# Performance work log

Measured on AMD Instinct MI355X. Metric: run time of the kernel, lower is better.

Reference implementation:

```python
import jax, jax.numpy as jnp
import numpy as np
import math

D_MODEL = 1024
NUM_HEADS = 16
D_K = D_MODEL // NUM_HEADS
THETA = 10000.0
CONTEXT_LENGTH = 2048


def _rope_tables(seq_len):
    # freqs: [d_k/2]
    powers = jnp.arange(0, D_K, 2, dtype=jnp.float32) / D_K
    freqs = 1.0 / (THETA ** powers)
    t = jnp.arange(seq_len, dtype=jnp.float32)
    fm = jnp.outer(t, freqs)  # [s, d_k/2]
    return jnp.cos(fm), jnp.sin(fm)


def _apply_rope(x, cos, sin):
    # x: [b, h, s, d_k]; cos/sin: [s, d_k/2] broadcast to [1,1,s,d_k/2]
    c = cos[None, None, :, :].astype(x.dtype)
    s_ = sin[None, None, :, :].astype(x.dtype)
    xe = x[..., 0::2]
    xo = x[..., 1::2]
    oe = xe * c - xo * s_
    oo = xe * s_ + xo * c
    # interleave even/odd back
    out = jnp.stack([oe, oo], axis=-1).reshape(x.shape)
    return out


def setup_inputs() -> dict:
    key = jax.random.key(0)
    ks = jax.random.split(key, 5)
    b, s = 4, 2048
    std = (2.0 / (D_MODEL + D_MODEL)) ** 0.5
    x = jax.random.normal(ks[0], (b, s, D_MODEL), dtype=jnp.float32)
    Wq = jax.random.normal(ks[1], (D_MODEL, D_MODEL), dtype=jnp.float32) * std
    Wk = jax.random.normal(ks[2], (D_MODEL, D_MODEL), dtype=jnp.float32) * std
    Wv = jax.random.normal(ks[3], (D_MODEL, D_MODEL), dtype=jnp.float32) * std
    Wo = jax.random.normal(ks[4], (D_MODEL, D_MODEL), dtype=jnp.float32) * std
    return {"x": x, "Wq": Wq, "Wk": Wk, "Wv": Wv, "Wo": Wo}


def reference(x, Wq, Wk, Wv, Wo):
    b, s, d = x.shape
    h, dk = NUM_HEADS, D_K
    # projections: Linear applies x @ W.T via einsum('...i,oi->...o')
    def proj(W):
        y = jnp.einsum('bsi,oi->bso', x, W)
        return y.reshape(b, s, h, dk).transpose(0, 2, 1, 3)  # [b,h,s,dk]
    q, k, v = proj(Wq), proj(Wk), proj(Wv)
    cos, sin = _rope_tables(s)
    q = _apply_rope(q, cos, sin)
    k = _apply_rope(k, cos, sin)
    scores = jnp.einsum('bhnd,bhmd->bhnm', q, k) / math.sqrt(dk)
    causal = jnp.tril(jnp.ones((s, s), dtype=bool))
    scores = jnp.where(causal, scores, -jnp.inf)
    probs = jax.nn.softmax(scores, axis=-1)
    attn = jnp.einsum('bhnm,bhmd->bhnd', probs, v)
    attn = attn.transpose(0, 2, 1, 3).reshape(b, s, d)  # [b,s,d_model]
    return jnp.einsum('bsi,oi->bso', attn, Wo)
```

## Files before the change

kernel.cpp:

```cpp
#include <hip/hip_runtime.h>
#include <hip/hip_bf16.h>
#include <math.h>

typedef __attribute__((ext_vector_type(4))) float f32x4;
typedef __attribute__((ext_vector_type(16))) float f32x16;
typedef __attribute__((ext_vector_type(8))) short s16x8;
typedef __attribute__((ext_vector_type(4))) unsigned u32x4;

#define LDSP(p) ((__attribute__((address_space(3))) void*)(p))
#define GLBP(p) ((const __attribute__((address_space(1))) void*)(p))

__device__ __forceinline__ unsigned short f2b(float f) {
  unsigned u = __builtin_bit_cast(unsigned, f);
  u += 0x7FFFu + ((u >> 16) & 1u);
  return (unsigned short)(u >> 16);
}
__device__ __forceinline__ float b2f(unsigned short h) {
  unsigned u = ((unsigned)h) << 16;
  return __builtin_bit_cast(float, u);
}
__device__ __forceinline__ unsigned cvtpk_bf16(float lo, float hi) {
  unsigned r;
  asm("v_cvt_pk_bf16_f32 %0, %1, %2" : "=v"(r) : "v"(lo), "v"(hi));
  return r;
}

__global__ void cvt_f2b_kernel(const float* __restrict__ src, unsigned short* __restrict__ dst, int n8) {
  int i = blockIdx.x * blockDim.x + threadIdx.x;
  if (i >= n8) return;
  const float4* s = (const float4*)src;
  float4 a = s[2 * i], b = s[2 * i + 1];
  s16x8 o;
  o[0] = (short)f2b(a.x); o[1] = (short)f2b(a.y); o[2] = (short)f2b(a.z); o[3] = (short)f2b(a.w);
  o[4] = (short)f2b(b.x); o[5] = (short)f2b(b.y); o[6] = (short)f2b(b.z); o[7] = (short)f2b(b.w);
  ((s16x8*)dst)[i] = o;
}

__global__ void rope_table_kernel(float* __restrict__ cosT, float* __restrict__ sinT) {
  int idx = blockIdx.x * 256 + threadIdx.x;
  int s = idx >> 5, j = idx & 31;
  float freq = (float)(1.0 / pow(10000.0, (double)(2 * j) / 64.0));
  float fm = (float)s * freq;
  cosT[idx] = cosf(fm);
  sinT[idx] = sinf(fm);
}

__global__ void rope_apply_kernel(unsigned short* __restrict__ qk, const float* __restrict__ cosT,
                                  const float* __restrict__ sinT, float scale) {
  int i = blockIdx.x * 256 + threadIdx.x;
  int e = i * 8;
  int s = (e >> 6) & 2047;
  int jb = (e & 63) >> 1;
  s16x8 v = ((const s16x8*)qk)[i];
  float4 c = *(const float4*)(cosT + s * 32 + jb);
  float4 sn = *(const float4*)(sinT + s * 32 + jb);
  float cc[4] = {c.x, c.y, c.z, c.w}, ss[4] = {sn.x, sn.y, sn.z, sn.w};
  s16x8 o;
#pragma unroll
  for (int p = 0; p < 4; ++p) {
    float e_ = b2f((unsigned short)v[2 * p]);
    float o_ = b2f((unsigned short)v[2 * p + 1]);
    o[2 * p]     = (short)f2b((e_ * cc[p] - o_ * ss[p]) * scale);
    o[2 * p + 1] = (short)f2b((e_ * ss[p] + o_ * cc[p]) * scale);
  }
  ((s16x8*)qk)[i] = o;
}

template <int EPI>
__global__ void gemm_bt_kernel(const unsigned short* __restrict__ A, const unsigned short* __restrict__ B,
                               float* __restrict__ Cf, unsigned short* __restrict__ Cq,
                               unsigned short* __restrict__ Ck, unsigned short* __restrict__ Cv,
                               int M, int N, int K) {
  __shared__ __align__(16) unsigned short As[128 * 64];
  __shared__ __align__(16) unsigned short Bs[128 * 64];
  const int t = threadIdx.x;
  const int lane = t & 63, wave = t >> 6;
  const int wm = wave >> 1, wn = wave & 1;
  const int g = lane >> 4, q = lane & 15;
  const int m0 = blockIdx.x * 128, n0 = blockIdx.y * 128;
  const int srow = t >> 3;
  const int scol = (t & 7) << 4;
  f32x4 acc[4][4] = {};
  const int nkt = K >> 6;
  for (int kt = 0; kt < nkt; ++kt) {
    __syncthreads();
#pragma unroll
    for (int it = 0; it < 4; ++it) {
      int row = it * 32 + srow;
      int cg = scol ^ ((row & 7) << 4);
      const char* ga = (const char*)A + ((size_t)(m0 + row) * K + (kt << 6)) * 2 + cg;
      __builtin_amdgcn_global_load_lds(GLBP(ga), LDSP((char*)As + it * 4096 + wave * 1024), 16, 0, 0);
      const char* gb = (const char*)B + ((size_t)(n0 + row) * K + (kt << 6)) * 2 + cg;
      __builtin_amdgcn_global_load_lds(GLBP(gb), LDSP((char*)Bs + it * 4096 + wave * 1024), 16, 0, 0);
    }
    asm volatile("s_waitcnt vmcnt(0)" ::: "memory");
    __syncthreads();
#pragma unroll
    for (int kk = 0; kk < 2; ++kk) {
      const int colB = ((kk << 6) + (g << 4)) ^ ((q & 7) << 4);
      s16x8 af[4], bf[4];
#pragma unroll
      for (int x = 0; x < 4; ++x) {
        af[x] = *(const s16x8*)(As + (wm * 64 + x * 16 + q) * 64 + (colB >> 1));
        bf[x] = *(const s16x8*)(Bs + (wn * 64 + x * 16 + q) * 64 + (colB >> 1));
      }
#pragma unroll
      for (int mi = 0; mi < 4; ++mi)
#pragma unroll
        for (int ni = 0; ni < 4; ++ni)
          acc[mi][ni] = __builtin_amdgcn_mfma_f32_16x16x32_bf16(af[mi], bf[ni], acc[mi][ni], 0, 0, 0);
    }
  }
  if (EPI == 0) {
#pragma unroll
    for (int mi = 0; mi < 4; ++mi)
#pragma unroll
      for (int r = 0; r < 4; ++r) {
        int m = m0 + wm * 64 + mi * 16 + g * 4 + r;
#pragma unroll
        for (int ni = 0; ni < 4; ++ni) {
          int n = n0 + wn * 64 + ni * 16 + q;
          Cf[(size_t)m * N + n] = acc[mi][ni][r];
        }
      }
  } else {
    unsigned short* dst = (n0 < 1024) ? Cq : (n0 < 2048 ? Ck : Cv);
    const int obase = n0 & 1023;
#pragma unroll
    for (int mi = 0; mi < 4; ++mi)
#pragma unroll
      for (int r = 0; r < 4; ++r) {
        int m = m0 + wm * 64 + mi * 16 + g * 4 + r;
        int bb = m >> 11, s = m & 2047;
#pragma unroll
        for (int ni = 0; ni < 4; ++ni) {
          int o = obase + wn * 64 + ni * 16 + q;
          int hh = o >> 6, d = o & 63;
          dst[(((size_t)bb * 16 + hh) * 2048 + s) * 64 + d] = f2b(acc[mi][ni][r]);
        }
      }
  }
}

#define BUILD_PA(dst, SS, B) {                                        \
    unsigned X  = cvtpk_bf16(SS[B + 0], SS[B + 1]);                   \
    unsigned X2 = cvtpk_bf16(SS[B + 2], SS[B + 3]);                   \
    unsigned Y  = cvtpk_bf16(SS[B + 4], SS[B + 5]);                   \
    unsigned Y2 = cvtpk_bf16(SS[B + 6], SS[B + 7]);                   \
    asm volatile("v_permlane32_swap_b32 %0, %1" : "+v"(X), "+v"(Y));  \
    asm volatile("v_permlane32_swap_b32 %0, %1" : "+v"(X2), "+v"(Y2));\
    u32x4 pw_; pw_[0] = X; pw_[1] = X2; pw_[2] = Y; pw_[3] = Y2;      \
    dst = __builtin_bit_cast(s16x8, pw_); }

__global__ void attn_kernel(const unsigned short* __restrict__ Q, const unsigned short* __restrict__ K,
                            const unsigned short* __restrict__ V, unsigned short* __restrict__ O) {
  __shared__ __align__(16) unsigned short Ks[2][64 * 64];
  __shared__ __align__(16) unsigned short Vt[2][64 * 72];
  const int t = threadIdx.x;
  const int lane = t & 63, w = t >> 6;
  const int h = lane >> 5, ql = lane & 31;
  const int bh = blockIdx.x;
  const int qt = 15 - (int)blockIdx.y;
  const size_t hoff = (size_t)bh * 2048 * 64;
  const int q_global = qt * 128 + w * 32 + ql;
  const int qmax_w = qt * 128 + w * 32 + 31;

  s16x8 qf[4];
  {
    const unsigned short* qp = Q + hoff + (size_t)q_global * 64 + h * 8;
#pragma unroll
    for (int s = 0; s < 4; ++s) qf[s] = *(const s16x8*)(qp + 16 * s);
  }
  f32x16 accO[2] = {};
  float mrun = -3e38f, lrun = 0.f;

  const int srow = t >> 3, scol = (t & 7) << 4;
  const int kv0 = 2 * (lane & 31);
  const int dbase = w * 16 + (lane >> 5) * 8;
  const int ntk = 2 * qt + 2;
  s16x8 va = {}, vb2 = {};

  for (int it = 0; it <= ntk; ++it) {
    const int buf = it & 1;
    if (it < ntk) {
      const char* kbp = (const char*)(K + hoff) + (size_t)it * 8192;
#pragma unroll
      for (int p = 0; p < 2; ++p) {
        int row = p * 32 + srow;
        int cg = scol ^ ((row & 7) << 4);
        __builtin_amdgcn_global_load_lds(GLBP(kbp + row * 128 + cg),
                                         LDSP((char*)Ks[buf] + p * 4096 + w * 1024), 16, 0, 0);
      }
      const unsigned short* vbp = V + hoff + (size_t)it * 4096;
      va  = *(const s16x8*)(vbp + kv0 * 64 + dbase);
      vb2 = *(const s16x8*)(vbp + (kv0 + 1) * 64 + dbase);
    }
    const int tkc = it - 1;
    if (tkc >= 0 && tkc * 64 <= qmax_w) {
      const int cb2 = tkc & 1;
      f32x16 S0 = {}, S1 = {};
      __builtin_amdgcn_s_setprio(1);
#pragma unroll
      for (int s = 0; s < 4; ++s) {
        const int cb = 16 * h + 32 * s;
        const int sw = (ql & 7) << 4;
        s16x8 kf0 = *(const s16x8*)((const char*)Ks[cb2] + ql * 128 + (cb ^ sw));
        S0 = __builtin_amdgcn_mfma_f32_32x32x16_bf16(kf0, qf[s], S0, 0, 0, 0);
        s16x8 kf1 = *(const s16x8*)((const char*)Ks[cb2] + (32 + ql) * 128 + (cb ^ sw));
        S1 = __builtin_amdgcn_mfma_f32_32x32x16_bf16(kf1, qf[s], S1, 0, 0, 0);
      }
      __builtin_amdgcn_s_setprio(0);
      if (tkc * 64 + 63 > qt * 128 + w * 32) {
        const int kvb = tkc * 64 + 4 * h;
#pragma unroll
        for (int r = 0; r < 16; ++r) {
          const int kvl = (r & 3) + 8 * (r >> 2);
          if (kvb + kvl > q_global) S0[r] = -3e38f;
          if (kvb + 32 + kvl > q_global) S1[r] = -3e38f;
        }
      }
      float pm = -3e38f;
#pragma unroll
      for (int r = 0; r < 16; ++r) pm = fmaxf(pm, fmaxf(S0[r], S1[r]));
      pm = fmaxf(pm, __shfl_xor(pm, 32));
      if (!__all(pm - mrun <= 8.0f)) {
        const float mnew = fmaxf(mrun, pm);
        const float alpha = exp2f(mrun - mnew);
        lrun *= alpha;
#pragma unroll
        for (int r = 0; r < 16; ++r) {
          float ar = __shfl(alpha, 4 * h + (r & 3) + 8 * (r >> 2));
          accO[0][r] *= ar;
          accO[1][r] *= ar;
        }
        mrun = mnew;
      }
      float ladd = 0.f;
#pragma unroll
      for (int r = 0; r < 16; ++r) {
        float p0 = exp2f(S0[r] - mrun);
        float p1 = exp2f(S1[r] - mrun);
        S0[r] = p0; S1[r] = p1;
        ladd += p0 + p1;
      }
      ladd += __shfl_xor(ladd, 32);
      lrun += ladd;
      s16x8 pa[4];
      BUILD_PA(pa[0], S0, 0);
      BUILD_PA(pa[1], S0, 8);
      BUILD_PA(pa[2], S1, 0);
      BUILD_PA(pa[3], S1, 8);
      __builtin_amdgcn_s_setprio(1);
#pragma unroll
      for (int s = 0; s < 4; ++s) {
#pragma unroll
        for (int dt = 0; dt < 2; ++dt) {
          s16x8 vf = *(const s16x8*)(Vt[cb2] + (dt * 32 + ql) * 72 + 8 * h + 16 * s);
          accO[dt] = __builtin_amdgcn_mfma_f32_32x32x16_bf16(pa[s], vf, accO[dt], 0, 0, 0);
        }
      }
      __builtin_amdgcn_s_setprio(0);
    }
    asm volatile("s_waitcnt vmcnt(0)" ::: "memory");
    if (it < ntk) {
#pragma unroll
      for (int j = 0; j < 8; ++j) {
        unsigned pk = (unsigned)(unsigned short)va[j] | ((unsigned)(unsigned short)vb2[j] << 16);
        *(unsigned*)((char*)Vt[buf] + (size_t)((dbase + j) * 72 + kv0) * 2) = pk;
      }
    }
    __syncthreads();
  }
  const float linv = 1.0f / lrun;
  const int bb = bh >> 4, hh = bh & 15;
#pragma unroll
  for (int r = 0; r < 16; ++r) {
    const int qrow = 4 * h + (r & 3) + 8 * (r >> 2);
    const float lr = __shfl(linv, qrow);
    const int sg = qt * 128 + w * 32 + qrow;
    const size_t base = ((size_t)(bb * 2048 + sg)) * 1024 + hh * 64 + ql;
    O[base] = f2b(accO[0][r] * lr);
    O[base + 32] = f2b(accO[1][r] * lr);
  }
}

extern "C" void kernel_launch(void* const* d_in, const int* in_sizes, int n_in,
                              void* d_out, int out_size, void* d_ws, size_t ws_size,
                              hipStream_t stream) {
  const float* x  = (const float*)d_in[0];
  const float* Wq = (const float*)d_in[1];
  const float* Wk = (const float*)d_in[2];
  const float* Wv = (const float*)d_in[3];
  const float* Wo = (const float*)d_in[4];
  char* ws = (char*)d_ws;
  unsigned short* xb   = (unsigned short*)(ws);
  unsigned short* wqkv = (unsigned short*)(ws + 16777216);
  unsigned short* wo   = (unsigned short*)(ws + 23068672);
  unsigned short* qb   = (unsigned short*)(ws + 25165824);
  unsigned short* kb   = (unsigned short*)(ws + 41943040);
  unsigned short* vb   = (unsigned short*)(ws + 58720256);
  unsigned short* ab   = (unsigned short*)(ws + 75497472);
  float* cosT = (float*)(ws + 92274688);
  float* sinT = (float*)(ws + 92536832);

  cvt_f2b_kernel<<<4096, 256, 0, stream>>>(x, xb, 1048576);
  cvt_f2b_kernel<<<512, 256, 0, stream>>>(Wq, wqkv, 131072);
  cvt_f2b_kernel<<<512, 256, 0, stream>>>(Wk, wqkv + 1048576, 131072);
  cvt_f2b_kernel<<<512, 256, 0, stream>>>(Wv, wqkv + 2097152, 131072);
  cvt_f2b_kernel<<<512, 256, 0, stream>>>(Wo, wo, 131072);
  rope_table_kernel<<<256, 256, 0, stream>>>(cosT, sinT);
  gemm_bt_kernel<1><<<dim3(64, 24), 256, 0, stream>>>(xb, wqkv, nullptr, qb, kb, vb, 8192, 3072, 1024);
  rope_apply_kernel<<<4096, 256, 0, stream>>>(qb, cosT, sinT, 0.125f * 1.44269504f);
  rope_apply_kernel<<<4096, 256, 0, stream>>>(kb, cosT, sinT, 1.0f);
  attn_kernel<<<dim3(64, 16), 256, 0, stream>>>(qb, kb, vb, ab);
  gemm_bt_kernel<0><<<dim3(64, 8), 256, 0, stream>>>(ab, wo, (float*)d_out, nullptr, nullptr, nullptr, 8192, 1024, 1024);
}
```

Before: 272.7 us.

## Rewrite GEMMs with 256x128 tiles, double-buffered LDS and XCD-aware block remap

Replaces the 128x128 single-buffered GEMM with a 256x128-tile kernel using 512 threads. It double-buffers the LDS so the next K-tile's global-to-LDS loads overlap the current tile's MFMA work. It remaps block IDs across the 8 XCDs for better L2 locality and raises wave priority around the MFMA bursts. The LDS footprint grows to 96KB per block, which may limit occupancy, and the remap hardcodes 32 M-tiles (M=8192).

```diff
diff --git a/kernel.cpp b/kernel.cpp
--- a/kernel.cpp
+++ b/kernel.cpp
@@ -67,59 +67,89 @@
 }
 
 template <int EPI>
-__global__ void gemm_bt_kernel(const unsigned short* __restrict__ A, const unsigned short* __restrict__ B,
-                               float* __restrict__ Cf, unsigned short* __restrict__ Cq,
-                               unsigned short* __restrict__ Ck, unsigned short* __restrict__ Cv,
-                               int M, int N, int K) {
-  __shared__ __align__(16) unsigned short As[128 * 64];
-  __shared__ __align__(16) unsigned short Bs[128 * 64];
+__global__ __launch_bounds__(512, 2) void gemm256_kernel(
+    const unsigned short* __restrict__ A, const unsigned short* __restrict__ B,
+    float* __restrict__ Cf, unsigned short* __restrict__ Cq,
+    unsigned short* __restrict__ Ck, unsigned short* __restrict__ Cv,
+    int M, int N, int K) {
+  __shared__ __align__(16) unsigned short As[2][256 * 64];
+  __shared__ __align__(16) unsigned short Bs[2][128 * 64];
   const int t = threadIdx.x;
-  const int lane = t & 63, wave = t >> 6;
-  const int wm = wave >> 1, wn = wave & 1;
+  const int lane = t & 63;
+  const int w = t >> 6;
+  const int wm = w >> 2, wn = w & 3;
   const int g = lane >> 4, q = lane & 15;
-  const int m0 = blockIdx.x * 128, n0 = blockIdx.y * 128;
+  const int nwg = gridDim.x;
+  const int bid = blockIdx.x;
+  const int sid = (bid & 7) * (nwg >> 3) + (bid >> 3);
+  const int m0 = (sid & 31) * 256;
+  const int n0 = (sid >> 5) * 128;
   const int srow = t >> 3;
   const int scol = (t & 7) << 4;
-  f32x4 acc[4][4] = {};
+  const size_t rbA = (size_t)K * 2;
+
+  f32x4 acc[8][2] = {};
   const int nkt = K >> 6;
+
+  auto stage = [&](int b, int kt) {
+    const size_t kof = (size_t)kt * 128;
+#pragma unroll
+    for (int p = 0; p < 4; ++p) {
+      int row = p * 64 + srow;
+      int cg = scol ^ ((row & 7) << 4);
+      const char* ga = (const char*)A + (size_t)(m0 + row) * rbA + kof + cg;
+      __builtin_amdgcn_global_load_lds(GLBP(ga), LDSP((char*)As[b] + p * 8192 + t * 16), 16, 0, 0);
+    }
+#pragma unroll
+    for (int p = 0; p < 2; ++p) {
+      int row = p * 64 + srow;
+      int cg = scol ^ ((row & 7) << 4);
+      const char* gb = (const char*)B + (size_t)(n0 + row) * rbA + kof + cg;
+      __builtin_amdgcn_global_load_lds(GLBP(gb), LDSP((char*)Bs[b] + p * 8192 + t * 16), 16, 0, 0);
+    }
+  };
+
+  stage(0, 0);
+  asm volatile("s_waitcnt vmcnt(0)" ::: "memory");
+  __syncthreads();
+
   for (int kt = 0; kt < nkt; ++kt) {
-    __syncthreads();
-#pragma unroll
-    for (int it = 0; it < 4; ++it) {
-      int row = it * 32 + srow;
-      int cg = scol ^ ((row & 7) << 4);
-      const char* ga = (const char*)A + ((size_t)(m0 + row) * K + (kt << 6)) * 2 + cg;
-      __builtin_amdgcn_global_load_lds(GLBP(ga), LDSP((char*)As + it * 4096 + wave * 1024), 16, 0, 0);
-      const char* gb = (const char*)B + ((size_t)(n0 + row) * K + (kt << 6)) * 2 + cg;
-      __builtin_amdgcn_global_load_lds(GLBP(gb), LDSP((char*)Bs + it * 4096 + wave * 1024), 16, 0, 0);
+    const int cur = kt & 1;
+    if (kt + 1 < nkt) stage(cur ^ 1, kt + 1);
+    const char* ab = (const char*)As[cur];
+    const char* bb = (const char*)Bs[cur];
+    const int sw = (q & 7) << 4;
+#pragma unroll
+    for (int kk = 0; kk < 2; ++kk) {
+      const int cb = kk * 64 + g * 16;
+      s16x8 bf[2], af[8];
+#pragma unroll
+      for (int ni = 0; ni < 2; ++ni)
+        bf[ni] = *(const s16x8*)(bb + (wn * 32 + ni * 16 + q) * 128 + (cb ^ sw));
+#pragma unroll
+      for (int mi = 0; mi < 8; ++mi)
+        af[mi] = *(const s16x8*)(ab + (wm * 128 + mi * 16 + q) * 128 + (cb ^ sw));
+      __builtin_amdgcn_s_setprio(1);
+#pragma unroll
+      for (int mi = 0; mi < 8; ++mi)
+#pragma unroll
+        for (int ni = 0; ni < 2; ++ni)
+          acc[mi][ni] = __builtin_amdgcn_mfma_f32_16x16x32_bf16(af[mi], bf[ni], acc[mi][ni], 0, 0, 0);
+      __builtin_amdgcn_s_setprio(0);
     }
     asm volatile("s_waitcnt vmcnt(0)" ::: "memory");
     __syncthreads();
-#pragma unroll
-    for (int kk = 0; kk < 2; ++kk) {
-      const int colB = ((kk << 6) + (g << 4)) ^ ((q & 7) << 4);
-      s16x8 af[4], bf[4];
-#pragma unroll
-      for (int x = 0; x < 4; ++x) {
-        af[x] = *(const s16x8*)(As + (wm * 64 + x * 16 + q) * 64 + (colB >> 1));
-        bf[x] = *(const s16x8*)(Bs + (wn * 64 + x * 16 + q) * 64 + (colB >> 1));
-      }
-#pragma unroll
-      for (int mi = 0; mi < 4; ++mi)
-#pragma unroll
-        for (int ni = 0; ni < 4; ++ni)
-          acc[mi][ni] = __builtin_amdgcn_mfma_f32_16x16x32_bf16(af[mi], bf[ni], acc[mi][ni], 0, 0, 0);
-    }
-  }
+  }
+
   if (EPI == 0) {
 #pragma unroll
-    for (int mi = 0; mi < 4; ++mi)
+    for (int mi = 0; mi < 8; ++mi)
 #pragma unroll
       for (int r = 0; r < 4; ++r) {
-        int m = m0 + wm * 64 + mi * 16 + g * 4 + r;
-#pragma unroll
-        for (int ni = 0; ni < 4; ++ni) {
-          int n = n0 + wn * 64 + ni * 16 + q;
+        int m = m0 + wm * 128 + mi * 16 + g * 4 + r;
+#pragma unroll
+        for (int ni = 0; ni < 2; ++ni) {
+          int n = n0 + wn * 32 + ni * 16 + q;
           Cf[(size_t)m * N + n] = acc[mi][ni][r];
         }
       }
@@ -127,16 +157,16 @@
     unsigned short* dst = (n0 < 1024) ? Cq : (n0 < 2048 ? Ck : Cv);
     const int obase = n0 & 1023;
 #pragma unroll
-    for (int mi = 0; mi < 4; ++mi)
+    for (int mi = 0; mi < 8; ++mi)
 #pragma unroll
       for (int r = 0; r < 4; ++r) {
-        int m = m0 + wm * 64 + mi * 16 + g * 4 + r;
-        int bb = m >> 11, s = m & 2047;
-#pragma unroll
-        for (int ni = 0; ni < 4; ++ni) {
-          int o = obase + wn * 64 + ni * 16 + q;
+        int m = m0 + wm * 128 + mi * 16 + g * 4 + r;
+        int bb2 = m >> 11, s = m & 2047;
+#pragma unroll
+        for (int ni = 0; ni < 2; ++ni) {
+          int o = obase + wn * 32 + ni * 16 + q;
           int hh = o >> 6, d = o & 63;
-          dst[(((size_t)bb * 16 + hh) * 2048 + s) * 64 + d] = f2b(acc[mi][ni][r]);
+          dst[(((size_t)bb2 * 16 + hh) * 2048 + s) * 64 + d] = f2b(acc[mi][ni][r]);
         }
       }
   }
@@ -309,9 +339,9 @@
   cvt_f2b_kernel<<<512, 256, 0, stream>>>(Wv, wqkv + 2097152, 131072);
   cvt_f2b_kernel<<<512, 256, 0, stream>>>(Wo, wo, 131072);
   rope_table_kernel<<<256, 256, 0, stream>>>(cosT, sinT);
-  gemm_bt_kernel<1><<<dim3(64, 24), 256, 0, stream>>>(xb, wqkv, nullptr, qb, kb, vb, 8192, 3072, 1024);
+  gemm256_kernel<1><<<768, 512, 0, stream>>>(xb, wqkv, nullptr, qb, kb, vb, 8192, 3072, 1024);
   rope_apply_kernel<<<4096, 256, 0, stream>>>(qb, cosT, sinT, 0.125f * 1.44269504f);
   rope_apply_kernel<<<4096, 256, 0, stream>>>(kb, cosT, sinT, 1.0f);
   attn_kernel<<<dim3(64, 16), 256, 0, stream>>>(qb, kb, vb, ab);
-  gemm_bt_kernel<0><<<dim3(64, 8), 256, 0, stream>>>(ab, wo, (float*)d_out, nullptr, nullptr, nullptr, 8192, 1024, 1024);
-}
+  gemm256_kernel<0><<<256, 512, 0, stream>>>(ab, wo, (float*)d_out, nullptr, nullptr, nullptr, 8192, 1024, 1024);
+}
```

Measured after the change: 296.6 us. +8.8%, slower.

## Rewrite projection GEMMs as 8-wave double-buffered kernel with interleaved prefetch

Applied to the files above, without the earlier changes.

Replaces the 4-wave 128x128 GEMM with an 8-wave kernel using 256-row tiles and a templated N tile (192 for QKV, 128 for output). LDS is double-buffered so the next K-tile's global-to-LDS loads are issued in phases between MFMA groups. Workgroup IDs are remapped across XCDs, and s_setprio is raised around MFMA blocks. This targets the exposed load latency and barrier stalls of the single-buffered loop, at the cost of more LDS and registers per block, which can limit occupancy.

```diff
diff --git a/kernel.cpp b/kernel.cpp
--- a/kernel.cpp
+++ b/kernel.cpp
@@ -66,51 +66,91 @@
   ((s16x8*)qk)[i] = o;
 }
 
-template <int EPI>
-__global__ void gemm_bt_kernel(const unsigned short* __restrict__ A, const unsigned short* __restrict__ B,
-                               float* __restrict__ Cf, unsigned short* __restrict__ Cq,
-                               unsigned short* __restrict__ Ck, unsigned short* __restrict__ Cv,
-                               int M, int N, int K) {
-  __shared__ __align__(16) unsigned short As[128 * 64];
-  __shared__ __align__(16) unsigned short Bs[128 * 64];
+template <int EPI, int NI>
+__global__ __launch_bounds__(512, 2) void gemm8p_kernel(
+    const unsigned short* __restrict__ A, const unsigned short* __restrict__ B,
+    float* __restrict__ Cf, unsigned short* __restrict__ Cq,
+    unsigned short* __restrict__ Ck, unsigned short* __restrict__ Cv,
+    int M, int N, int K) {
+  constexpr int BN = 32 * NI;
+  __shared__ __align__(16) unsigned short Asm[2][256 * 64];
+  __shared__ __align__(16) unsigned short Bsm[2][BN * 64];
   const int t = threadIdx.x;
-  const int lane = t & 63, wave = t >> 6;
-  const int wm = wave >> 1, wn = wave & 1;
+  const int lane = t & 63, w = t >> 6;
+  const int wm = w >> 1, wn = w & 1;
   const int g = lane >> 4, q = lane & 15;
-  const int m0 = blockIdx.x * 128, n0 = blockIdx.y * 128;
-  const int srow = t >> 3;
-  const int scol = (t & 7) << 4;
-  f32x4 acc[4][4] = {};
+  const int nwg = gridDim.x, bid = blockIdx.x;
+  const int sid = (bid & 7) * (nwg >> 3) + (bid >> 3);
+  const int nnt = N / BN;
+  const int m0 = (sid / nnt) * 256;
+  const int n0 = (sid % nnt) * BN;
+  const size_t rb = (size_t)K * 2;
+  const int l3 = lane >> 3, l7 = lane & 7;
+  const int scg = (l7 << 4) ^ (l3 << 4);
+
+  f32x4 acc[4][NI] = {};
   const int nkt = K >> 6;
+
+  auto stageA = [&](int b, int p, int kt2) {
+    int row = p * 64 + w * 8 + l3;
+    const char* gp = (const char*)A + (size_t)(m0 + row) * rb + (size_t)kt2 * 128 + scg;
+    __builtin_amdgcn_global_load_lds(GLBP(gp), LDSP((char*)Asm[b] + p * 8192 + w * 1024), 16, 0, 0);
+  };
+  auto stageB = [&](int b, int p, int kt2) {
+    int row = p * 64 + w * 8 + l3;
+    const char* gp = (const char*)B + (size_t)(n0 + row) * rb + (size_t)kt2 * 128 + scg;
+    __builtin_amdgcn_global_load_lds(GLBP(gp), LDSP((char*)Bsm[b] + p * 8192 + w * 1024), 16, 0, 0);
+  };
+
+#pragma unroll
+  for (int p = 0; p < 4; ++p) stageA(0, p, 0);
+#pragma unroll
+  for (int p = 0; p < NI / 2; ++p) stageB(0, p, 0);
+  asm volatile("s_waitcnt vmcnt(0)" ::: "memory");
+  asm volatile("s_barrier" ::: "memory");
+
   for (int kt = 0; kt < nkt; ++kt) {
-    __syncthreads();
-#pragma unroll
-    for (int it = 0; it < 4; ++it) {
-      int row = it * 32 + srow;
-      int cg = scol ^ ((row & 7) << 4);
-      const char* ga = (const char*)A + ((size_t)(m0 + row) * K + (kt << 6)) * 2 + cg;
-      __builtin_amdgcn_global_load_lds(GLBP(ga), LDSP((char*)As + it * 4096 + wave * 1024), 16, 0, 0);
-      const char* gb = (const char*)B + ((size_t)(n0 + row) * K + (kt << 6)) * 2 + cg;
-      __builtin_amdgcn_global_load_lds(GLBP(gb), LDSP((char*)Bs + it * 4096 + wave * 1024), 16, 0, 0);
+    const int cur = kt & 1;
+    const bool pf = kt + 1 < nkt;
+    const char* ab = (const char*)Asm[cur];
+    const char* bb = (const char*)Bsm[cur];
+    const int sw = (q & 7) << 4;
+    s16x8 afr[4], bfr[NI / 2];
+#pragma unroll
+    for (int kk = 0; kk < 2; ++kk) {
+#pragma unroll
+      for (int nh = 0; nh < 2; ++nh) {
+        const int cb = (kk * 64 + g * 16) ^ sw;
+        if (nh == 0) {
+#pragma unroll
+          for (int mi = 0; mi < 4; ++mi)
+            afr[mi] = *(const s16x8*)(ab + (wm * 64 + mi * 16 + q) * 128 + cb);
+        }
+#pragma unroll
+        for (int j = 0; j < NI / 2; ++j)
+          bfr[j] = *(const s16x8*)(bb + (wn * (NI * 16) + (nh * (NI / 2) + j) * 16 + q) * 128 + cb);
+        const int ph = kk * 2 + nh;
+        if (pf) {
+          if (ph == 0)      { stageA(cur ^ 1, 0, kt + 1); stageA(cur ^ 1, 1, kt + 1); }
+          else if (ph == 1) { stageA(cur ^ 1, 2, kt + 1); stageA(cur ^ 1, 3, kt + 1); }
+          else if (ph == 2) { stageB(cur ^ 1, 0, kt + 1); if (NI / 2 > 1) stageB(cur ^ 1, 1, kt + 1); }
+          else              { if (NI / 2 > 2) stageB(cur ^ 1, 2, kt + 1); }
+        }
+        asm volatile("s_barrier" ::: "memory");
+        __builtin_amdgcn_s_setprio(1);
+#pragma unroll
+        for (int mi = 0; mi < 4; ++mi)
+#pragma unroll
+          for (int j = 0; j < NI / 2; ++j)
+            acc[mi][nh * (NI / 2) + j] =
+                __builtin_amdgcn_mfma_f32_16x16x32_bf16(afr[mi], bfr[j], acc[mi][nh * (NI / 2) + j], 0, 0, 0);
+        __builtin_amdgcn_s_setprio(0);
+        if (ph == 3) asm volatile("s_waitcnt vmcnt(0)" ::: "memory");
+        asm volatile("s_barrier" ::: "memory");
+      }
     }
-    asm volatile("s_waitcnt vmcnt(0)" ::: "memory");
-    __syncthreads();
-#pragma unroll
-    for (int kk = 0; kk < 2; ++kk) {
-      const int colB = ((kk << 6) + (g << 4)) ^ ((q & 7) << 4);
-      s16x8 af[4], bf[4];
-#pragma unroll
-      for (int x = 0; x < 4; ++x) {
-        af[x] = *(const s16x8*)(As + (wm * 64 + x * 16 + q) * 64 + (colB >> 1));
-        bf[x] = *(const s16x8*)(Bs + (wn * 64 + x * 16 + q) * 64 + (colB >> 1));
-      }
-#pragma unroll
-      for (int mi = 0; mi < 4; ++mi)
-#pragma unroll
-        for (int ni = 0; ni < 4; ++ni)
-          acc[mi][ni] = __builtin_amdgcn_mfma_f32_16x16x32_bf16(af[mi], bf[ni], acc[mi][ni], 0, 0, 0);
-    }
-  }
+  }
+
   if (EPI == 0) {
 #pragma unroll
     for (int mi = 0; mi < 4; ++mi)
@@ -118,25 +158,25 @@
       for (int r = 0; r < 4; ++r) {
         int m = m0 + wm * 64 + mi * 16 + g * 4 + r;
 #pragma unroll
-        for (int ni = 0; ni < 4; ++ni) {
-          int n = n0 + wn * 64 + ni * 16 + q;
+        for (int ni = 0; ni < NI; ++ni) {
+          int n = n0 + wn * (NI * 16) + ni * 16 + q;
           Cf[(size_t)m * N + n] = acc[mi][ni][r];
         }
       }
   } else {
-    unsigned short* dst = (n0 < 1024) ? Cq : (n0 < 2048 ? Ck : Cv);
-    const int obase = n0 & 1023;
 #pragma unroll
     for (int mi = 0; mi < 4; ++mi)
 #pragma unroll
       for (int r = 0; r < 4; ++r) {
         int m = m0 + wm * 64 + mi * 16 + g * 4 + r;
-        int bb = m >> 11, s = m & 2047;
-#pragma unroll
-        for (int ni = 0; ni < 4; ++ni) {
-          int o = obase + wn * 64 + ni * 16 + q;
-          int hh = o >> 6, d = o & 63;
-          dst[(((size_t)bb * 16 + hh) * 2048 + s) * 64 + d] = f2b(acc[mi][ni][r]);
+        int bb2 = m >> 11, s = m & 2047;
+#pragma unroll
+        for (int ni = 0; ni < NI; ++ni) {
+          int off = n0 + wn * (NI * 16) + ni * 16;
+          unsigned short* dst = (off < 1024) ? Cq : (off < 2048 ? Ck : Cv);
+          int o = off & 1023;
+          int hh = o >> 6, d = (o & 63) + q;
+          dst[(((size_t)bb2 * 16 + hh) * 2048 + s) * 64 + d] = f2b(acc[mi][ni][r]);
         }
       }
   }
@@ -309,9 +349,9 @@
   cvt_f2b_kernel<<<512, 256, 0, stream>>>(Wv, wqkv + 2097152, 131072);
   cvt_f2b_kernel<<<512, 256, 0, stream>>>(Wo, wo, 131072);
   rope_table_kernel<<<256, 256, 0, stream>>>(cosT, sinT);
-  gemm_bt_kernel<1><<<dim3(64, 24), 256, 0, stream>>>(xb, wqkv, nullptr, qb, kb, vb, 8192, 3072, 1024);
+  gemm8p_kernel<1, 6><<<512, 512, 0, stream>>>(xb, wqkv, nullptr, qb, kb, vb, 8192, 3072, 1024);
   rope_apply_kernel<<<4096, 256, 0, stream>>>(qb, cosT, sinT, 0.125f * 1.44269504f);
   rope_apply_kernel<<<4096, 256, 0, stream>>>(kb, cosT, sinT, 1.0f);
   attn_kernel<<<dim3(64, 16), 256, 0, stream>>>(qb, kb, vb, ab);
-  gemm_bt_kernel<0><<<dim3(64, 8), 256, 0, stream>>>(ab, wo, (float*)d_out, nullptr, nullptr, nullptr, 8192, 1024, 1024);
-}
+  gemm8p_kernel<0, 4><<<256, 512, 0, stream>>>(ab, wo, (float*)d_out, nullptr, nullptr, nullptr, 8192, 1024, 1024);
+}
```

New measurement: 276.2 us. About the same (+1.3%).
